# Kernel optimization log

Measured on AMD Instinct MI355X. Metric: run time of the kernel, lower is better.

## Reference

```python
import jax, jax.numpy as jnp
import numpy as np

B, S, D = 2, 1024, 4096
NQ, NKV, HD = 32, 8, 128
G = NQ // NKV
FFN = 10928  # ffn_size(4096, 4.0): int(4*4096)*2//3 = 10922 -> round up to mult of 8
ATTN_MULT = 0.08838834764831845
MAX_ATTN = 30.0
EPS = 1e-5
BASE = 10000.0


def setup_inputs() -> dict:
    key = jax.random.key(0)
    ks = jax.random.split(key, 13)
    def w(k, shape):
        return jax.random.normal(k, shape, jnp.float32) / np.float32(np.sqrt(shape[0]))
    return {
        "x": jax.random.normal(ks[0], (B, S, D), jnp.float32),
        "mask": jnp.tril(jnp.ones((1, 1, S, S), dtype=bool)),  # causal
        "scale_pre_attn": jax.random.uniform(ks[1], (D,), jnp.float32, 0.5, 1.5),
        "scale_post_attn": jax.random.uniform(ks[2], (D,), jnp.float32, 0.5, 1.5),
        "scale_pre_mlp": jax.random.uniform(ks[3], (D,), jnp.float32, 0.5, 1.5),
        "scale_post_mlp": jax.random.uniform(ks[4], (D,), jnp.float32, 0.5, 1.5),
        "wq": w(ks[5], (D, NQ * HD)),
        "wk": w(ks[6], (D, NKV * HD)),
        "wv": w(ks[7], (D, NKV * HD)),
        "wo": w(ks[8], (NQ * HD, D)),
        "w_gate": w(ks[9], (D, FFN)),
        "w_val": w(ks[10], (D, FFN)),
        "w_out": w(ks[11], (FFN, D)),
    }


def rms_norm(x, scale):
    ms = jnp.mean(jnp.square(x), axis=-1, keepdims=True)
    return x * jax.lax.rsqrt(ms + EPS) * scale


def rotate_half(x):
    x1, x2 = jnp.split(x, 2, axis=-1)
    return jnp.concatenate((-x2, x1), axis=-1)


def apply_rope(x):
    # x: [b, s, h, d]; offset=0 (no KV-cache step)
    s, d = x.shape[1], x.shape[3]
    inv_freq = 1.0 / (BASE ** (jnp.arange(0, d, 2, dtype=jnp.float32) / d))
    t = jnp.arange(s, dtype=jnp.float32)
    phase = t[:, None] * inv_freq[None, :]            # [s, d/2]
    phase = jnp.tile(phase, (1, 2))[None, :, None, :]  # [1, s, 1, d]
    return (x * jnp.cos(phase) + rotate_half(x) * jnp.sin(phase)).astype(x.dtype)


def reference(x, mask, scale_pre_attn, scale_post_attn, scale_pre_mlp, scale_post_mlp,
              wq, wk, wv, wo, w_gate, w_val, w_out):
    h = x
    # ---- attention sublayer (pre-norm) ----
    hn = rms_norm(h, scale_pre_attn)
    q = (hn @ wq).reshape(B, S, NQ, HD)
    k = (hn @ wk).reshape(B, S, NKV, HD)
    v = (hn @ wv).reshape(B, S, NKV, HD)
    q = apply_rope(q)
    k = apply_rope(k)
    qg = q.reshape(B, S, NKV, G, HD)  # GQA: group q heads per kv head
    logits = jnp.einsum("btkgd,bskd->bkgts", qg, k).astype(jnp.float32) * ATTN_MULT
    logits = MAX_ATTN * jnp.tanh(logits / MAX_ATTN)   # grok soft cap
    logits = jnp.where(mask[:, :, None], logits, -1e30)
    probs = jax.nn.softmax(logits, axis=-1).astype(x.dtype)
    attn = jnp.einsum("bkgts,bskd->btkgd", probs, v).reshape(B, S, NQ * HD)
    h_attn = attn @ wo
    h = h + rms_norm(h_attn, scale_post_attn)
    # ---- gated MLP sublayer (pre-norm) ----
    hn2 = rms_norm(h, scale_pre_mlp)
    h_dense = (jax.nn.gelu(hn2 @ w_gate) * (hn2 @ w_val)) @ w_out
    h = h + rms_norm(h_dense, scale_post_mlp)
    return h
```

## Files before the change

### kernel.cpp

```cpp
#include <hip/hip_runtime.h>
#include <stdint.h>

typedef unsigned short ushort_t;
typedef __bf16 bf16x8 __attribute__((ext_vector_type(8)));
typedef float f32x4 __attribute__((ext_vector_type(4)));

#define D_MODEL 4096
#define SEQ 1024
#define BROWS 2048
#define QKV_N 6144
#define HD 128
#define FFN_PAD 10944
#define FFN_GRID 11008
#define ATTN_MULT 0.08838834764831845f

__device__ __forceinline__ unsigned short f2bf(float f){
  union { float f; unsigned u; } c; c.f = f;
  unsigned u = c.u + 0x7fffu + ((c.u >> 16) & 1u);
  return (unsigned short)(u >> 16);
}
__device__ __forceinline__ float bf2f(unsigned short h){
  union { unsigned u; float f; } c; c.u = ((unsigned)h) << 16;
  return c.f;
}
__device__ __forceinline__ f32x4 zero4(){ f32x4 z; z[0]=0.f; z[1]=0.f; z[2]=0.f; z[3]=0.f; return z; }
__device__ __forceinline__ bf16x8 ldb8(const void* p){ return *(const bf16x8*)p; }
__device__ __forceinline__ f32x4 MFMA(bf16x8 a, bf16x8 b, f32x4 c){
  return __builtin_amdgcn_mfma_f32_16x16x32_bf16(a, b, c, 0, 0, 0);
}
__device__ __forceinline__ void g2lds16(void* lds, const void* g){
  __builtin_amdgcn_global_load_lds(
      (const __attribute__((address_space(1))) void*)(uintptr_t)(g),
      (__attribute__((address_space(3))) void*)(uint32_t)(uintptr_t)(lds),
      16, 0, 0);
}
#define BAR() __builtin_amdgcn_s_barrier()
#define VMCNT6() asm volatile("s_waitcnt vmcnt(6)" ::: "memory")
#define VMCNT8() asm volatile("s_waitcnt vmcnt(8)" ::: "memory")
#define VMCNT0() asm volatile("s_waitcnt vmcnt(0)" ::: "memory")
#define LGKM0() asm volatile("s_waitcnt lgkmcnt(0)" ::: "memory")

__global__ __launch_bounds__(256) void rmsnorm_in(const float* __restrict__ x,
                                                  const float* __restrict__ sc,
                                                  ushort_t* __restrict__ out){
  int row = blockIdx.x, tid = threadIdx.x;
  const float4* xr = (const float4*)(x + (size_t)row*D_MODEL);
  float4 v[4]; float ss = 0.f;
#pragma unroll
  for (int i=0;i<4;i++){
    v[i] = xr[tid + i*256];
    ss += v[i].x*v[i].x + v[i].y*v[i].y + v[i].z*v[i].z + v[i].w*v[i].w;
  }
#pragma unroll
  for (int m=32;m;m>>=1) ss += __shfl_xor(ss, m);
  __shared__ float red[4];
  if ((tid&63)==0) red[tid>>6] = ss;
  __syncthreads();
  float inv = rsqrtf((red[0]+red[1]+red[2]+red[3])*(1.f/4096.f) + 1e-5f);
  const float4* scv = (const float4*)sc;
#pragma unroll
  for (int i=0;i<4;i++){
    float4 s4 = scv[tid + i*256];
    ushort4 o;
    o.x = f2bf(v[i].x*inv*s4.x); o.y = f2bf(v[i].y*inv*s4.y);
    o.z = f2bf(v[i].z*inv*s4.z); o.w = f2bf(v[i].w*inv*s4.w);
    ((ushort4*)out)[(size_t)row*1024 + tid + i*256] = o;
  }
}

__global__ __launch_bounds__(256) void rmsnorm_resid(const float* __restrict__ base,
                                                     const float* __restrict__ delta,
                                                     const float* __restrict__ sc1,
                                                     float* __restrict__ hout,
                                                     const float* __restrict__ sc2,
                                                     ushort_t* __restrict__ hn2){
  int row = blockIdx.x, tid = threadIdx.x;
  const float4* dr = (const float4*)(delta + (size_t)row*D_MODEL);
  const float4* br = (const float4*)(base  + (size_t)row*D_MODEL);
  float4 d[4]; float ss = 0.f;
#pragma unroll
  for (int i=0;i<4;i++){
    d[i] = dr[tid + i*256];
    ss += d[i].x*d[i].x + d[i].y*d[i].y + d[i].z*d[i].z + d[i].w*d[i].w;
  }
#pragma unroll
  for (int m=32;m;m>>=1) ss += __shfl_xor(ss, m);
  __shared__ float red[4];
  if ((tid&63)==0) red[tid>>6] = ss;
  __syncthreads();
  float inv1 = rsqrtf((red[0]+red[1]+red[2]+red[3])*(1.f/4096.f) + 1e-5f);
  const float4* s1v = (const float4*)sc1;
  float4* ho = (float4*)(hout + (size_t)row*D_MODEL);
  float4 h4[4]; float ss2 = 0.f;
#pragma unroll
  for (int i=0;i<4;i++){
    float4 b4 = br[tid + i*256];
    float4 s4 = s1v[tid + i*256];
    float4 h;
    h.x = b4.x + d[i].x*inv1*s4.x;
    h.y = b4.y + d[i].y*inv1*s4.y;
    h.z = b4.z + d[i].z*inv1*s4.z;
    h.w = b4.w + d[i].w*inv1*s4.w;
    h4[i] = h;
    ho[tid + i*256] = h;
    ss2 += h.x*h.x + h.y*h.y + h.z*h.z + h.w*h.w;
  }
  if (sc2){
#pragma unroll
    for (int m=32;m;m>>=1) ss2 += __shfl_xor(ss2, m);
    __syncthreads();
    if ((tid&63)==0) red[tid>>6] = ss2;
    __syncthreads();
    float inv2 = rsqrtf((red[0]+red[1]+red[2]+red[3])*(1.f/4096.f) + 1e-5f);
    const float4* s2v = (const float4*)sc2;
#pragma unroll
    for (int i=0;i<4;i++){
      float4 s4 = s2v[tid + i*256];
      ushort4 o;
      o.x = f2bf(h4[i].x*inv2*s4.x); o.y = f2bf(h4[i].y*inv2*s4.y);
      o.z = f2bf(h4[i].z*inv2*s4.z); o.w = f2bf(h4[i].w*inv2*s4.w);
      ((ushort4*)hn2)[(size_t)row*1024 + tid + i*256] = o;
    }
  }
}

__global__ __launch_bounds__(256) void convT(const float* __restrict__ W,
                                             ushort_t* __restrict__ WT,
                                             int K, int N, int Kp, int Np){
  __shared__ float tile[64][65];
  int n0 = blockIdx.x*64, k0 = blockIdx.y*64;
  int tx = threadIdx.x & 63, ty = threadIdx.x >> 6;
#pragma unroll
  for (int i=0;i<16;i++){
    int k = k0 + ty + i*4, n = n0 + tx;
    tile[ty+i*4][tx] = (k < K && n < N) ? W[(size_t)k*N + n] : 0.f;
  }
  __syncthreads();
  int wtx = threadIdx.x & 15, wty = threadIdx.x >> 4;
#pragma unroll
  for (int j=0;j<4;j++){
    int n = n0 + wty + j*16;
    if (n < Np){
      ushort4 o;
      o.x = f2bf(tile[wtx*4+0][wty + j*16]);
      o.y = f2bf(tile[wtx*4+1][wty + j*16]);
      o.z = f2bf(tile[wtx*4+2][wty + j*16]);
      o.w = f2bf(tile[wtx*4+3][wty + j*16]);
      *(ushort4*)&WT[(size_t)n*Kp + k0 + wtx*4] = o;
    }
  }
}

template<int MODE>
__global__ __launch_bounds__(512, 2) void gemm256(const ushort_t* __restrict__ A, int lda,
                                                  const ushort_t* __restrict__ WT, int ldw,
                                                  void* __restrict__ Cv, int ldc,
                                                  int Nvalid, int K){
  __shared__ __align__(16) char smem[147456];
  const int nwg = gridDim.x;
  const int lid = blockIdx.x;
  const int t  = (lid & 7) * (nwg >> 3) + (lid >> 3);
  const int m0 = (t & 7) << 8;
  const int n0 = (t >> 3) << 7;
  const int tid = threadIdx.x;
  const int w = tid >> 6, lane = tid & 63;
  const int wm = w >> 1, wn = w & 1;
  const int lo = lane & 15, hi = lane >> 4;
  const int srow = lane >> 3, scol = lane & 7;
  const int sw = scol ^ srow;
  const int rsw = lo & 7;
  const int NT = K >> 6;

  const ushort_t* pA = A  + (size_t)(m0 + w*8 + srow) * lda + sw*8;
  const ushort_t* pB = WT + (size_t)(n0 + w*8 + srow) * ldw + sw*8;

  auto stage = [&](int tt, int slot, int c){
    const ushort_t* g = (c < 4 ? pA + (size_t)(c*64)*lda : pB + (size_t)((c-4)*64)*ldw) + (size_t)tt*64;
    char* l = smem + slot*49152 + (c < 4 ? c*8192 : 32768 + (c-4)*8192) + (w<<10);
    g2lds16(l, g);
  };

  f32x4 acc[4][4];
#pragma unroll
  for (int i=0;i<4;i++)
#pragma unroll
    for (int j=0;j<4;j++) acc[i][j] = zero4();

#pragma unroll
  for (int c=0;c<6;c++) stage(0, 0, c);
#pragma unroll
  for (int c=0;c<6;c++) stage(1, 1, c);

  int cur = 0;
  for (int i=0;i<NT;i++){
    if (i == NT-1) VMCNT0(); else VMCNT6();
    BAR();
    const char* sA = smem + cur*49152;
    const char* sB = sA + 32768;
    const int nxt = (cur == 2) ? 0 : cur + 1;
    const int nn  = (nxt == 2) ? 0 : nxt + 1;
    if (i+2 < NT){
      stage(i+2, nn, 0); stage(i+2, nn, 1); stage(i+2, nn, 2);
      stage(i+2, nn, 3); stage(i+2, nn, 4); stage(i+2, nn, 5);
    }
    bf16x8 af[4][2], bfr[4][2];
#pragma unroll
    for (int rf=0;rf<4;rf++)
#pragma unroll
      for (int kc=0;kc<2;kc++)
        af[rf][kc] = ldb8(sA + (wm*64 + rf*16 + lo)*128 + (((kc*4+hi)^rsw)<<4));
#pragma unroll
    for (int cf=0;cf<4;cf++)
#pragma unroll
      for (int kc=0;kc<2;kc++)
        bfr[cf][kc] = ldb8(sB + (wn*64 + cf*16 + lo)*128 + (((kc*4+hi)^rsw)<<4));
#pragma unroll
    for (int rf=0;rf<4;rf++)
#pragma unroll
      for (int cf=0;cf<4;cf++)
#pragma unroll
        for (int kc=0;kc<2;kc++)
          acc[rf][cf] = MFMA(af[rf][kc], bfr[cf][kc], acc[rf][cf]);
    cur = nxt;
  }
#pragma unroll
  for (int rf=0;rf<4;rf++){
#pragma unroll
    for (int cf=0;cf<4;cf++){
#pragma unroll
      for (int r=0;r<4;r++){
        int m = m0 + wm*64 + rf*16 + hi*4 + r;
        int n = n0 + wn*64 + cf*16 + lo;
        if (n < Nvalid){
          float v = acc[rf][cf][r];
          size_t idx = (size_t)m*ldc + n;
          if (MODE == 1) ((float*)Cv)[idx] = v;
          else           ((ushort_t*)Cv)[idx] = f2bf(v);
        }
      }
    }
  }
}

__global__ __launch_bounds__(512, 2) void gemm_gv(const ushort_t* __restrict__ A, int lda,
                                                  const ushort_t* __restrict__ B1,
                                                  const ushort_t* __restrict__ B2, int ldw,
                                                  ushort_t* __restrict__ Cv, int ldc,
                                                  int Nvalid, int K){
  __shared__ __align__(16) char smem[131072];
  const int nwg = gridDim.x;
  const int lid = blockIdx.x;
  const int t  = (lid & 7) * (nwg >> 3) + (lid >> 3);
  const int m0 = (t & 7) << 8;
  const int n0 = (t >> 3) << 7;
  const int tid = threadIdx.x;
  const int w = tid >> 6, lane = tid & 63;
  const int wm = w >> 1, wn = w & 1;
  const int lo = lane & 15, hi = lane >> 4;
  const int srow = lane >> 3, scol = lane & 7;
  const int sw = scol ^ srow;
  const int rsw = lo & 7;
  const int NT = K >> 6;

  const ushort_t* pA  = A  + (size_t)(m0 + w*8 + srow) * lda + sw*8;
  const ushort_t* pB1 = B1 + (size_t)(n0 + w*8 + srow) * ldw + sw*8;
  const ushort_t* pB2 = B2 + (size_t)(n0 + w*8 + srow) * ldw + sw*8;

  auto stage = [&](int tt, int c){
    const ushort_t* g;
    int lofs;
    if (c < 4){ g = pA  + (size_t)(c*64)*lda;     lofs = c*8192; }
    else if (c < 6){ g = pB1 + (size_t)((c-4)*64)*ldw; lofs = 32768 + (c-4)*8192; }
    else { g = pB2 + (size_t)((c-6)*64)*ldw; lofs = 49152 + (c-6)*8192; }
    g2lds16(smem + ((tt&1)<<16) + lofs + (w<<10), g + (size_t)tt*64);
  };

  f32x4 ag[4][4], av[4][4];
#pragma unroll
  for (int i=0;i<4;i++)
#pragma unroll
    for (int j=0;j<4;j++){ ag[i][j] = zero4(); av[i][j] = zero4(); }

#pragma unroll
  for (int c=0;c<8;c++) stage(0, c);
#pragma unroll
  for (int c=0;c<8;c++) stage(1, c);

  for (int i=0;i<NT;i++){
    if (i == NT-1) VMCNT0(); else VMCNT8();
    BAR();
    const char* sA  = smem + ((i&1)<<16);
    const char* sB1 = sA + 32768;
    const char* sB2 = sA + 49152;
    bf16x8 af[4][2], b1f[4][2], b2f[4][2];
#pragma unroll
    for (int rf=0;rf<4;rf++)
#pragma unroll
      for (int kc=0;kc<2;kc++)
        af[rf][kc] = ldb8(sA + (wm*64 + rf*16 + lo)*128 + (((kc*4+hi)^rsw)<<4));
#pragma unroll
    for (int cf=0;cf<4;cf++)
#pragma unroll
      for (int kc=0;kc<2;kc++){
        b1f[cf][kc] = ldb8(sB1 + (wn*64 + cf*16 + lo)*128 + (((kc*4+hi)^rsw)<<4));
        b2f[cf][kc] = ldb8(sB2 + (wn*64 + cf*16 + lo)*128 + (((kc*4+hi)^rsw)<<4));
      }
    LGKM0();
    BAR();
    if (i+2 < NT){
#pragma unroll
      for (int c=0;c<8;c++) stage(i+2, c);
    }
#pragma unroll
    for (int rf=0;rf<4;rf++)
#pragma unroll
      for (int cf=0;cf<4;cf++)
#pragma unroll
        for (int kc=0;kc<2;kc++){
          ag[rf][cf] = MFMA(af[rf][kc], b1f[cf][kc], ag[rf][cf]);
          av[rf][cf] = MFMA(af[rf][kc], b2f[cf][kc], av[rf][cf]);
        }
  }
#pragma unroll
  for (int rf=0;rf<4;rf++){
#pragma unroll
    for (int cf=0;cf<4;cf++){
#pragma unroll
      for (int r=0;r<4;r++){
        int m = m0 + wm*64 + rf*16 + hi*4 + r;
        int n = n0 + wn*64 + cf*16 + lo;
        if (n < Nvalid){
          float g = ag[rf][cf][r];
          float v = av[rf][cf][r];
          float ga = 0.5f*g*(1.f + tanhf(0.7978845608028654f*(g + 0.044715f*g*g*g)));
          Cv[(size_t)m*ldc + n] = f2bf(ga * v);
        }
      }
    }
  }
}

__global__ void rope_tab_kernel(float* __restrict__ tab){
  int s = blockIdx.x, i = threadIdx.x;
  float invf = __expf(-(float)i * (9.210340371976184f/64.f));
  float ph = (float)s * invf;
  float sn, cs;
  sincosf(ph, &sn, &cs);
  tab[s*128 + i] = cs;
  tab[s*128 + 64 + i] = sn;
}

__global__ __launch_bounds__(256) void rope_apply(ushort_t* __restrict__ qkv,
                                                  const float* __restrict__ tab){
  int idx = blockIdx.x*256 + threadIdx.x;
  int pr = idx & 63;
  int h  = (idx >> 6) % 40;
  int row = idx / 2560;
  int t = row & (SEQ-1);
  ushort_t* p = qkv + (size_t)row*QKV_N + h*HD + pr;
  float c = tab[t*128 + pr], s = tab[t*128 + 64 + pr];
  float x1 = bf2f(p[0]), x2 = bf2f(p[64]);
  p[0]  = f2bf(x1*c - x2*s);
  p[64] = f2bf(x2*c + x1*s);
}

__global__ __launch_bounds__(256) void transpose_v(const ushort_t* __restrict__ qkv,
                                                   ushort_t* __restrict__ VT){
  __shared__ ushort_t tile[32][33];
  int d0 = blockIdx.x*32, m0 = blockIdx.y*32;
  int tx = threadIdx.x & 31, ty = threadIdx.x >> 5;
#pragma unroll
  for (int i=0;i<4;i++)
    tile[ty + i*8][tx] = qkv[(size_t)(m0 + ty + i*8)*QKV_N + 5120 + d0 + tx];
  __syncthreads();
#pragma unroll
  for (int i=0;i<4;i++)
    VT[(size_t)(d0 + ty + i*8)*BROWS + m0 + tx] = tile[tx][ty + i*8];
}

__global__ __launch_bounds__(256) void attn_kernel(const ushort_t* __restrict__ qkv,
                                                   const ushort_t* __restrict__ VT,
                                                   ushort_t* __restrict__ outp){
  const int blk = blockIdx.x;
  const int bh = blk & 63;
  const int tgrp = 15 - (blk >> 6);
  const int b = bh >> 5, qh = bh & 31, kv = qh >> 2;
  const int w = threadIdx.x >> 6, lane = threadIdx.x & 63;
  const int lo = lane & 15, hi = lane >> 4;
  const int t0 = tgrp*64 + w*16;
  __shared__ ushort_t P[4][16][72];
  ushort_t (*Pw)[72] = P[w];

  const ushort_t* Qb = qkv + (size_t)(b*SEQ + t0 + lo)*QKV_N + qh*HD + hi*8;
  bf16x8 qf[4];
#pragma unroll
  for (int c=0;c<4;c++) qf[c] = ldb8(Qb + c*32);

  f32x4 of[8];
#pragma unroll
  for (int i=0;i<8;i++) of[i] = zero4();
  float ls[4] = {0.f,0.f,0.f,0.f};

  const ushort_t* Kb = qkv + (size_t)(b*SEQ + lo)*QKV_N + D_MODEL + kv*HD + hi*8;
  const ushort_t* Vb = VT + (size_t)(kv*HD + lo)*BROWS + b*SEQ + hi*8;

  const int nst = tgrp + 1;
  for (int st=0; st<nst; st++){
    const int s0 = st*64;
    f32x4 sacc[4];
#pragma unroll
    for (int nf=0;nf<4;nf++) sacc[nf] = zero4();
#pragma unroll
    for (int c=0;c<4;c++){
#pragma unroll
      for (int nf=0;nf<4;nf++){
        bf16x8 kf = ldb8(Kb + (size_t)(s0 + nf*16)*QKV_N + c*32);
        sacc[nf] = MFMA(qf[c], kf, sacc[nf]);
      }
    }
#pragma unroll
    for (int nf=0;nf<4;nf++){
#pragma unroll
      for (int r=0;r<4;r++){
        int tq = t0 + hi*4 + r;
        int s = s0 + nf*16 + lo;
        float xx = sacc[nf][r] * ATTN_MULT;
        float z = fminf(fmaxf(xx*(2.f/30.f), -80.f), 80.f);
        float e = __expf(z);
        float th = (e - 1.f)/(e + 1.f);
        float p = (s <= tq) ? __expf(30.f*th - 30.f) : 0.f;
        ls[r] += p;
        Pw[hi*4+r][nf*16+lo] = f2bf(p);
      }
    }
    __builtin_amdgcn_sched_barrier(0);
    __builtin_amdgcn_s_waitcnt(0xc07f);
    __builtin_amdgcn_sched_barrier(0);
#pragma unroll
    for (int c2=0;c2<2;c2++){
      bf16x8 pf = ldb8(&Pw[lo][c2*32 + hi*8]);
#pragma unroll
      for (int nf2=0;nf2<8;nf2++){
        bf16x8 vf = ldb8(Vb + (size_t)(nf2*16)*BROWS + s0 + c2*32);
        of[nf2] = MFMA(pf, vf, of[nf2]);
      }
    }
    __builtin_amdgcn_sched_barrier(0);
  }
#pragma unroll
  for (int m=1;m<16;m<<=1){
#pragma unroll
    for (int r=0;r<4;r++) ls[r] += __shfl_xor(ls[r], m);
  }
  float inv[4];
#pragma unroll
  for (int r=0;r<4;r++) inv[r] = 1.f/ls[r];
  ushort_t* Ob = outp + (size_t)(b*SEQ + t0 + hi*4)*D_MODEL + qh*HD + lo;
#pragma unroll
  for (int nf2=0;nf2<8;nf2++)
#pragma unroll
    for (int r=0;r<4;r++)
      Ob[(size_t)r*D_MODEL + nf2*16] = f2bf(of[nf2][r]*inv[r]);
}

extern "C" void kernel_launch(void* const* d_in, const int* in_sizes, int n_in,
                              void* d_out, int out_size, void* d_ws, size_t ws_size,
                              hipStream_t stream){
  const float* x        = (const float*)d_in[0];
  const float* sc_pre_a = (const float*)d_in[2];
  const float* sc_post_a= (const float*)d_in[3];
  const float* sc_pre_m = (const float*)d_in[4];
  const float* sc_post_m= (const float*)d_in[5];
  const float* wq  = (const float*)d_in[6];
  const float* wk  = (const float*)d_in[7];
  const float* wv  = (const float*)d_in[8];
  const float* wo  = (const float*)d_in[9];
  const float* wg  = (const float*)d_in[10];
  const float* wva = (const float*)d_in[11];
  const float* wou = (const float*)d_in[12];

  char* ws = (char*)d_ws;
  size_t off = 0;
  auto alloc = [&](size_t bytes)->void*{
    void* p = ws + off; off += (bytes + 255) & ~(size_t)255; return p;
  };
  ushort_t* WT   = (ushort_t*)alloc((size_t)FFN_GRID*D_MODEL*2);
  ushort_t* hn   = (ushort_t*)alloc((size_t)BROWS*D_MODEL*2);
  ushort_t* qkv  = (ushort_t*)alloc((size_t)BROWS*QKV_N*2);
  ushort_t* VT   = (ushort_t*)alloc((size_t)SEQ*BROWS*2);
  ushort_t* attn = (ushort_t*)alloc((size_t)BROWS*D_MODEL*2);
  float*    tmp32= (float*)alloc((size_t)BROWS*D_MODEL*4);
  ushort_t* hn2  = (ushort_t*)alloc((size_t)BROWS*D_MODEL*2);
  ushort_t* act  = (ushort_t*)alloc((size_t)BROWS*FFN_PAD*2);
  float*    rtab = (float*)alloc((size_t)SEQ*128*4);
  float* h = (float*)d_out;
  ushort_t* WT2  = (ushort_t*)hn;

  rmsnorm_in<<<BROWS, 256, 0, stream>>>(x, sc_pre_a, hn);
  convT<<<dim3(64, 64), 256, 0, stream>>>(wq, WT,                     4096, 4096, 4096, 4096);
  convT<<<dim3(16, 64), 256, 0, stream>>>(wk, WT + (size_t)4096*4096, 4096, 1024, 4096, 1024);
  convT<<<dim3(16, 64), 256, 0, stream>>>(wv, WT + (size_t)5120*4096, 4096, 1024, 4096, 1024);
  gemm256<0><<<384, 512, 0, stream>>>(hn, 4096, WT, 4096, qkv, QKV_N, QKV_N, 4096);
  rope_tab_kernel<<<SEQ, 64, 0, stream>>>(rtab);
  rope_apply<<<(BROWS*40*64)/256, 256, 0, stream>>>(qkv, rtab);
  transpose_v<<<dim3(32,64), 256, 0, stream>>>(qkv, VT);
  attn_kernel<<<1024, 256, 0, stream>>>(qkv, VT, attn);
  convT<<<dim3(64, 64), 256, 0, stream>>>(wo, WT, 4096, 4096, 4096, 4096);
  gemm256<1><<<256, 512, 0, stream>>>(attn, 4096, WT, 4096, tmp32, 4096, 4096, 4096);
  rmsnorm_resid<<<BROWS, 256, 0, stream>>>(x, tmp32, sc_post_a, h, sc_pre_m, hn2);
  convT<<<dim3(172, 64), 256, 0, stream>>>(wg,  WT,  4096, 10928, 4096, FFN_GRID);
  convT<<<dim3(172, 64), 256, 0, stream>>>(wva, WT2, 4096, 10928, 4096, FFN_GRID);
  gemm_gv<<<688, 512, 0, stream>>>(hn2, 4096, WT, WT2, 4096, act, FFN_PAD, FFN_PAD, 4096);
  convT<<<dim3(64, 171), 256, 0, stream>>>(wou, WT, 10928, 4096, FFN_PAD, 4096);
  gemm256<1><<<256, 512, 0, stream>>>(act, FFN_PAD, WT, FFN_PAD, tmp32, 4096, 4096, FFN_PAD);
  rmsnorm_resid<<<BROWS, 256, 0, stream>>>(h, tmp32, sc_post_m, h, nullptr, nullptr);
}
```

Measured before the change: 1.211 ms.

## Use 256x256 GEMM tiles with double buffering and split-K for output projections

The GEMM kernel is generalised to 256x256 output tiles per workgroup. Staging moves from a three-slot ring to a two-slot double buffer, with an extra LDS-drain barrier before the next prefetch is issued. The attention output and MLP down projections use split-K=2, writing two fp32 partials that the following RMSNorm/residual kernel sums, so enough workgroups stay busy despite the larger tiles. The FFN padding grows to 11008 so the K range splits evenly. Risks are more accumulator registers per thread, the extra barrier shrinking load/compute overlap, and partial buffers aliased onto reused workspace (part_u overruns hn into the qkv region).

```diff
diff --git a/kernel.cpp b/kernel.cpp
--- a/kernel.cpp
+++ b/kernel.cpp
@@ -10,7 +10,6 @@
 #define BROWS 2048
 #define QKV_N 6144
 #define HD 128
-#define FFN_PAD 10944
 #define FFN_GRID 11008
 #define ATTN_MULT 0.08838834764831845f
 
@@ -35,7 +34,6 @@
       16, 0, 0);
 }
 #define BAR() __builtin_amdgcn_s_barrier()
-#define VMCNT6() asm volatile("s_waitcnt vmcnt(6)" ::: "memory")
 #define VMCNT8() asm volatile("s_waitcnt vmcnt(8)" ::: "memory")
 #define VMCNT0() asm volatile("s_waitcnt vmcnt(0)" ::: "memory")
 #define LGKM0() asm volatile("s_waitcnt lgkmcnt(0)" ::: "memory")
@@ -70,17 +68,24 @@
 
 __global__ __launch_bounds__(256) void rmsnorm_resid(const float* __restrict__ base,
                                                      const float* __restrict__ delta,
+                                                     const float* __restrict__ delta2,
                                                      const float* __restrict__ sc1,
                                                      float* __restrict__ hout,
                                                      const float* __restrict__ sc2,
                                                      ushort_t* __restrict__ hn2){
   int row = blockIdx.x, tid = threadIdx.x;
   const float4* dr = (const float4*)(delta + (size_t)row*D_MODEL);
+  const float4* d2 = delta2 ? (const float4*)(delta2 + (size_t)row*D_MODEL) : nullptr;
   const float4* br = (const float4*)(base  + (size_t)row*D_MODEL);
   float4 d[4]; float ss = 0.f;
 #pragma unroll
   for (int i=0;i<4;i++){
-    d[i] = dr[tid + i*256];
+    float4 a = dr[tid + i*256];
+    if (d2){
+      float4 b = d2[tid + i*256];
+      a.x += b.x; a.y += b.y; a.z += b.z; a.w += b.w;
+    }
+    d[i] = a;
     ss += d[i].x*d[i].x + d[i].y*d[i].y + d[i].z*d[i].z + d[i].w*d[i].w;
   }
 #pragma unroll
@@ -151,17 +156,22 @@
   }
 }
 
-template<int MODE>
-__global__ __launch_bounds__(512, 2) void gemm256(const ushort_t* __restrict__ A, int lda,
-                                                  const ushort_t* __restrict__ WT, int ldw,
-                                                  void* __restrict__ Cv, int ldc,
-                                                  int Nvalid, int K){
-  __shared__ __align__(16) char smem[147456];
+template<int MODE, int KS>
+__global__ __launch_bounds__(512, 2) void gemmW(const ushort_t* __restrict__ A, int lda,
+                                                const ushort_t* __restrict__ WT, int ldw,
+                                                void* __restrict__ Cv, void* __restrict__ Cv2,
+                                                int ldc, int Nvalid, int K){
+  __shared__ __align__(16) char smem[131072];
   const int nwg = gridDim.x;
   const int lid = blockIdx.x;
-  const int t  = (lid & 7) * (nwg >> 3) + (lid >> 3);
+  int t = (lid & 7) * (nwg >> 3) + (lid >> 3);
+  void* Cout = Cv;
+  if (KS == 2){
+    const int per = nwg >> 1;
+    if (t >= per){ t -= per; A += (size_t)K; WT += (size_t)K; Cout = Cv2; }
+  }
   const int m0 = (t & 7) << 8;
-  const int n0 = (t >> 3) << 7;
+  const int n0 = (t >> 3) << 8;
   const int tid = threadIdx.x;
   const int w = tid >> 6, lane = tid & 63;
   const int wm = w >> 1, wn = w & 1;
@@ -174,68 +184,65 @@
   const ushort_t* pA = A  + (size_t)(m0 + w*8 + srow) * lda + sw*8;
   const ushort_t* pB = WT + (size_t)(n0 + w*8 + srow) * ldw + sw*8;
 
-  auto stage = [&](int tt, int slot, int c){
+  auto stage = [&](int tt, int c){
     const ushort_t* g = (c < 4 ? pA + (size_t)(c*64)*lda : pB + (size_t)((c-4)*64)*ldw) + (size_t)tt*64;
-    char* l = smem + slot*49152 + (c < 4 ? c*8192 : 32768 + (c-4)*8192) + (w<<10);
-    g2lds16(l, g);
+    g2lds16(smem + ((tt&1)<<16) + (c < 4 ? c*8192 : 32768 + (c-4)*8192) + (w<<10), g);
   };
 
-  f32x4 acc[4][4];
+  f32x4 acc[4][8];
 #pragma unroll
   for (int i=0;i<4;i++)
 #pragma unroll
-    for (int j=0;j<4;j++) acc[i][j] = zero4();
-
-#pragma unroll
-  for (int c=0;c<6;c++) stage(0, 0, c);
-#pragma unroll
-  for (int c=0;c<6;c++) stage(1, 1, c);
-
-  int cur = 0;
+    for (int j=0;j<8;j++) acc[i][j] = zero4();
+
+#pragma unroll
+  for (int c=0;c<8;c++) stage(0, c);
+#pragma unroll
+  for (int c=0;c<8;c++) stage(1, c);
+
   for (int i=0;i<NT;i++){
-    if (i == NT-1) VMCNT0(); else VMCNT6();
+    if (i == NT-1) VMCNT0(); else VMCNT8();
     BAR();
-    const char* sA = smem + cur*49152;
+    const char* sA = smem + ((i&1)<<16);
     const char* sB = sA + 32768;
-    const int nxt = (cur == 2) ? 0 : cur + 1;
-    const int nn  = (nxt == 2) ? 0 : nxt + 1;
-    if (i+2 < NT){
-      stage(i+2, nn, 0); stage(i+2, nn, 1); stage(i+2, nn, 2);
-      stage(i+2, nn, 3); stage(i+2, nn, 4); stage(i+2, nn, 5);
-    }
-    bf16x8 af[4][2], bfr[4][2];
+    bf16x8 af[4][2], bfr[8][2];
 #pragma unroll
     for (int rf=0;rf<4;rf++)
 #pragma unroll
       for (int kc=0;kc<2;kc++)
         af[rf][kc] = ldb8(sA + (wm*64 + rf*16 + lo)*128 + (((kc*4+hi)^rsw)<<4));
 #pragma unroll
-    for (int cf=0;cf<4;cf++)
+    for (int cf=0;cf<8;cf++)
 #pragma unroll
       for (int kc=0;kc<2;kc++)
-        bfr[cf][kc] = ldb8(sB + (wn*64 + cf*16 + lo)*128 + (((kc*4+hi)^rsw)<<4));
+        bfr[cf][kc] = ldb8(sB + (wn*128 + cf*16 + lo)*128 + (((kc*4+hi)^rsw)<<4));
+    LGKM0();
+    BAR();
+    if (i+2 < NT){
+#pragma unroll
+      for (int c=0;c<8;c++) stage(i+2, c);
+    }
 #pragma unroll
     for (int rf=0;rf<4;rf++)
 #pragma unroll
-      for (int cf=0;cf<4;cf++)
+      for (int cf=0;cf<8;cf++)
 #pragma unroll
         for (int kc=0;kc<2;kc++)
           acc[rf][cf] = MFMA(af[rf][kc], bfr[cf][kc], acc[rf][cf]);
-    cur = nxt;
   }
 #pragma unroll
   for (int rf=0;rf<4;rf++){
 #pragma unroll
-    for (int cf=0;cf<4;cf++){
+    for (int cf=0;cf<8;cf++){
 #pragma unroll
       for (int r=0;r<4;r++){
         int m = m0 + wm*64 + rf*16 + hi*4 + r;
-        int n = n0 + wn*64 + cf*16 + lo;
+        int n = n0 + wn*128 + cf*16 + lo;
         if (n < Nvalid){
           float v = acc[rf][cf][r];
           size_t idx = (size_t)m*ldc + n;
-          if (MODE == 1) ((float*)Cv)[idx] = v;
-          else           ((ushort_t*)Cv)[idx] = f2bf(v);
+          if (MODE == 1) ((float*)Cout)[idx] = v;
+          else           ((ushort_t*)Cout)[idx] = f2bf(v);
         }
       }
     }
@@ -491,27 +498,29 @@
   ushort_t* attn = (ushort_t*)alloc((size_t)BROWS*D_MODEL*2);
   float*    tmp32= (float*)alloc((size_t)BROWS*D_MODEL*4);
   ushort_t* hn2  = (ushort_t*)alloc((size_t)BROWS*D_MODEL*2);
-  ushort_t* act  = (ushort_t*)alloc((size_t)BROWS*FFN_PAD*2);
+  ushort_t* act  = (ushort_t*)alloc((size_t)BROWS*FFN_GRID*2);
   float*    rtab = (float*)alloc((size_t)SEQ*128*4);
   float* h = (float*)d_out;
   ushort_t* WT2  = (ushort_t*)hn;
+  float* part_o  = (float*)act;
+  float* part_u  = (float*)hn;
 
   rmsnorm_in<<<BROWS, 256, 0, stream>>>(x, sc_pre_a, hn);
   convT<<<dim3(64, 64), 256, 0, stream>>>(wq, WT,                     4096, 4096, 4096, 4096);
   convT<<<dim3(16, 64), 256, 0, stream>>>(wk, WT + (size_t)4096*4096, 4096, 1024, 4096, 1024);
   convT<<<dim3(16, 64), 256, 0, stream>>>(wv, WT + (size_t)5120*4096, 4096, 1024, 4096, 1024);
-  gemm256<0><<<384, 512, 0, stream>>>(hn, 4096, WT, 4096, qkv, QKV_N, QKV_N, 4096);
+  gemmW<0,1><<<192, 512, 0, stream>>>(hn, 4096, WT, 4096, qkv, nullptr, QKV_N, QKV_N, 4096);
   rope_tab_kernel<<<SEQ, 64, 0, stream>>>(rtab);
   rope_apply<<<(BROWS*40*64)/256, 256, 0, stream>>>(qkv, rtab);
   transpose_v<<<dim3(32,64), 256, 0, stream>>>(qkv, VT);
   attn_kernel<<<1024, 256, 0, stream>>>(qkv, VT, attn);
   convT<<<dim3(64, 64), 256, 0, stream>>>(wo, WT, 4096, 4096, 4096, 4096);
-  gemm256<1><<<256, 512, 0, stream>>>(attn, 4096, WT, 4096, tmp32, 4096, 4096, 4096);
-  rmsnorm_resid<<<BROWS, 256, 0, stream>>>(x, tmp32, sc_post_a, h, sc_pre_m, hn2);
+  gemmW<1,2><<<256, 512, 0, stream>>>(attn, 4096, WT, 4096, tmp32, part_o, 4096, 4096, 2048);
+  rmsnorm_resid<<<BROWS, 256, 0, stream>>>(x, tmp32, part_o, sc_post_a, h, sc_pre_m, hn2);
   convT<<<dim3(172, 64), 256, 0, stream>>>(wg,  WT,  4096, 10928, 4096, FFN_GRID);
   convT<<<dim3(172, 64), 256, 0, stream>>>(wva, WT2, 4096, 10928, 4096, FFN_GRID);
-  gemm_gv<<<688, 512, 0, stream>>>(hn2, 4096, WT, WT2, 4096, act, FFN_PAD, FFN_PAD, 4096);
-  convT<<<dim3(64, 171), 256, 0, stream>>>(wou, WT, 10928, 4096, FFN_PAD, 4096);
-  gemm256<1><<<256, 512, 0, stream>>>(act, FFN_PAD, WT, FFN_PAD, tmp32, 4096, 4096, FFN_PAD);
-  rmsnorm_resid<<<BROWS, 256, 0, stream>>>(h, tmp32, sc_post_m, h, nullptr, nullptr);
-}
+  gemm_gv<<<688, 512, 0, stream>>>(hn2, 4096, WT, WT2, 4096, act, FFN_GRID, FFN_GRID, 4096);
+  convT<<<dim3(64, 172), 256, 0, stream>>>(wou, WT, 10928, 4096, FFN_GRID, 4096);
+  gemmW<1,2><<<256, 512, 0, stream>>>(act, FFN_GRID, WT, FFN_GRID, tmp32, part_u, 4096, 4096, 5504);
+  rmsnorm_resid<<<BROWS, 256, 0, stream>>>(h, tmp32, part_u, sc_post_m, h, nullptr, nullptr);
+}
```

After: 1.202 ms. Within noise of the previous version (-0.7%).
